# Optimization experiments

Measured on AMD Instinct MI355X. Metric: run time of the kernel, lower is better.

Reference implementation:

```python
import jax, jax.numpy as jnp
import numpy as np

T, B, DIM, N, K = 512, 32, 1024, 256, 32  # K = checkpoint interval, divides T


def setup_inputs() -> dict:
    key = jax.random.key(0)
    k1, k2, k3, k4 = jax.random.split(key, 4)
    scale = 1.0 / np.sqrt(DIM)  # keep projections O(1) like trained weights
    return {
        "x": jax.random.normal(k1, (T, B, DIM), dtype=jnp.float32),
        "S0": jnp.zeros((B, N, N), dtype=jnp.float32),
        "W_k": jax.random.normal(k2, (N, DIM), dtype=jnp.float32) * scale,
        "W_v": jax.random.normal(k3, (N, DIM), dtype=jnp.float32) * scale,
        "W_q": jax.random.normal(k4, (N, DIM), dtype=jnp.float32) * scale,
    }


def reference(x, S0, W_k, W_v, W_q):
    # Projections (batched GEMMs), done once up-front as in the torch code.
    k_all = jnp.einsum("tbd,nd->tbn", x, W_k)
    v_all = jnp.einsum("tbd,nd->tbn", x, W_v)
    q_all = jnp.einsum("tbd,nd->tbn", x, W_q)
    k_norm = k_all / (jnp.linalg.norm(k_all, axis=-1, keepdims=True) + 1e-6)

    def step(S, kvq):
        kn, v, q = kvq  # each [B, N]
        retrieved = jnp.einsum("bij,bj->bi", S, kn)          # S @ k_norm
        S = S + (v - retrieved)[:, :, None] * kn[:, None, :]  # rank-1 delta write
        Sq = jnp.einsum("bij,bj->bi", S, q)                   # readout with updated S
        out = Sq * jax.nn.silu(Sq)
        return S, out

    def segment(S, kvq_seg):
        return jax.lax.scan(step, S, kvq_seg)

    nseg = T // K
    seg_kvq = (
        k_norm.reshape(nseg, K, B, N),
        v_all.reshape(nseg, K, B, N),
        q_all.reshape(nseg, K, B, N),
    )
    _, outs = jax.lax.scan(segment, S0, seg_kvq)  # [nseg, K, B, N]
    return outs.reshape(T, B, N)
```

## Files before the change

kernel.cpp:

```cpp
#include <hip/hip_runtime.h>
#include <hip/hip_bf16.h>
#include <math.h>

#define T_DIM 512
#define B_DIM 32
#define D_DIM 1024
#define N_DIM 256
#define M_DIM (T_DIM * B_DIM)
#define CHUNK 32
#define NCHUNK (T_DIM / CHUNK)
#define IBLK 32
#define ST (B_DIM * N_DIM)
#define BK 32

typedef _Float16 f16;
typedef _Float16 f16x8 __attribute__((ext_vector_type(8)));
typedef _Float16 f16x4 __attribute__((ext_vector_type(4)));
typedef __fp16   h16x2 __attribute__((ext_vector_type(2)));
typedef float    f32x4 __attribute__((ext_vector_type(4)));

#define LDK 264
#define LDT 40
#define LDV 36

#define GLOAD_LDS16(g, l)                                         \
  __builtin_amdgcn_global_load_lds(                               \
      (const __attribute__((address_space(1))) void*)(g),         \
      (__attribute__((address_space(3))) void*)(l), 16, 0, 0)

__device__ __forceinline__ f16x8 cvt8(const float4& a, const float4& b) {
  f16x8 h;
  h[0] = (f16)a.x; h[1] = (f16)a.y; h[2] = (f16)a.z; h[3] = (f16)a.w;
  h[4] = (f16)b.x; h[5] = (f16)b.y; h[6] = (f16)b.z; h[7] = (f16)b.w;
  return h;
}

__device__ __forceinline__ f16x8 pk8(const f32x4 a, const f32x4 b) {
  union { f16x8 v; h16x2 p[4]; } u;
  u.p[0] = __builtin_amdgcn_cvt_pkrtz(a[0], a[1]);
  u.p[1] = __builtin_amdgcn_cvt_pkrtz(a[2], a[3]);
  u.p[2] = __builtin_amdgcn_cvt_pkrtz(b[0], b[1]);
  u.p[3] = __builtin_amdgcn_cvt_pkrtz(b[2], b[3]);
  return u.v;
}

__global__ __launch_bounds__(256) void cvt_w_kernel(
    const float* __restrict__ wk, const float* __restrict__ wv,
    const float* __restrict__ wq, f16* __restrict__ out) {
  const int i = (blockIdx.x * 256 + threadIdx.x) * 8;
  const int m = blockIdx.y;
  const float* src = (m == 0) ? wk : (m == 1) ? wv : wq;
  const float4 f0 = *(const float4*)(src + i);
  const float4 f1 = *(const float4*)(src + i + 4);
  *(f16x8*)(out + (size_t)m * (N_DIM * D_DIM) + i) = cvt8(f0, f1);
}

__global__ __launch_bounds__(256, 4) void proj_gemm_mfma(
    const float* __restrict__ x, const f16* __restrict__ Wh,
    f16* __restrict__ ok, f16* __restrict__ ov, f16* __restrict__ oq) {
  __shared__ __align__(16) float Af[128 * BK];
  __shared__ __align__(16) f16   Bh[128 * BK];

  const int tid  = threadIdx.x;
  const int lane = tid & 63;
  const int w    = tid >> 6;
  const int wm   = w >> 1, wn = w & 1;
  const int lr   = lane & 15;
  const int lq   = lane >> 4;

  const int mb  = blockIdx.x * 128;
  const int mat = blockIdx.y >> 1;
  const int nb  = (blockIdx.y & 1) * 128;

  const f16* Wmat = Wh + (size_t)mat * (N_DIM * D_DIM) + (size_t)nb * D_DIM;
  f16*       C    = (mat == 0) ? ok : (mat == 1) ? ov : oq;

  const int arow = 8 * w + (lane >> 3);
  const int acq  = (lane & 7) ^ (lane >> 3);
  const int brow = 16 * w + (lane >> 2);
  const int bco  = (lane & 3) ^ ((lane >> 3) & 3);

  const float* a_base = x + (size_t)mb * D_DIM;

  f32x4 acc[4][4];
  #pragma unroll
  for (int i = 0; i < 4; ++i)
    #pragma unroll
    for (int j = 0; j < 4; ++j) acc[i][j] = (f32x4){0.f, 0.f, 0.f, 0.f};

  for (int kt = 0; kt < D_DIM; kt += BK) {
    #pragma unroll
    for (int j = 0; j < 4; ++j) {
      const int r = 32 * j + arow;
      GLOAD_LDS16(a_base + (size_t)r * D_DIM + kt + acq * 4,
                  &Af[(32 * j + 8 * w) * BK]);
    }
    #pragma unroll
    for (int j = 0; j < 2; ++j) {
      const int r = 64 * j + brow;
      GLOAD_LDS16(Wmat + (size_t)r * D_DIM + kt + bco * 8,
                  &Bh[(64 * j + 16 * w) * BK]);
    }
    __syncthreads();

    f16x8 af[4], bf[4];
    #pragma unroll
    for (int mi = 0; mi < 4; ++mi) {
      const int row = 64 * wm + 16 * mi + lr;
      const int q0  = (2 * lq)     ^ (row & 7);
      const int q1  = (2 * lq + 1) ^ (row & 7);
      const f32x4 a0 = *(const f32x4*)&Af[row * BK + q0 * 4];
      const f32x4 a1 = *(const f32x4*)&Af[row * BK + q1 * 4];
      af[mi] = pk8(a0, a1);
    }
    #pragma unroll
    for (int nj = 0; nj < 4; ++nj) {
      const int row = 64 * wn + 16 * nj + lr;
      const int sp  = lq ^ ((lr >> 1) & 3);
      bf[nj] = *(const f16x8*)&Bh[row * BK + sp * 8];
    }
    #pragma unroll
    for (int mi = 0; mi < 4; ++mi)
      #pragma unroll
      for (int nj = 0; nj < 4; ++nj)
        acc[mi][nj] = __builtin_amdgcn_mfma_f32_16x16x32_f16(af[mi], bf[nj], acc[mi][nj], 0, 0, 0);
    __syncthreads();
  }

  #pragma unroll
  for (int mi = 0; mi < 4; ++mi)
    #pragma unroll
    for (int nj = 0; nj < 4; ++nj)
      #pragma unroll
      for (int r = 0; r < 4; ++r) {
        const int rg = mb + 64 * wm + 16 * mi + 4 * lq + r;
        const int cg = nb + 64 * wn + 16 * nj + lr;
        C[(size_t)rg * N_DIM + cg] = (f16)acc[mi][nj][r];
      }
}

__global__ __launch_bounds__(256) void knorm_kernel(f16* __restrict__ k) {
  const int w    = threadIdx.x >> 6;
  const int lane = threadIdx.x & 63;
  const int row  = blockIdx.x * 4 + w;
  f16* p = k + (size_t)row * N_DIM + lane * 4;
  f16x4 h = *reinterpret_cast<const f16x4*>(p);
  const float x0 = (float)h[0], x1 = (float)h[1], x2 = (float)h[2], x3 = (float)h[3];
  float ss = x0 * x0 + x1 * x1 + x2 * x2 + x3 * x3;
  #pragma unroll
  for (int m = 1; m < 64; m <<= 1) ss += __shfl_xor(ss, m, 64);
  const float inv = 1.0f / (sqrtf(ss) + 1e-6f);
  h[0] = (f16)(x0 * inv); h[1] = (f16)(x1 * inv);
  h[2] = (f16)(x2 * inv); h[3] = (f16)(x3 * inv);
  *reinterpret_cast<f16x4*>(p) = h;
}

__global__ __launch_bounds__(256, 2) void precompute_wg(
    const f16* __restrict__ kn, const f16* __restrict__ q,
    f16* __restrict__ Wg, f16* __restrict__ Gg, f16* __restrict__ KTg) {
  __shared__ __align__(16) f16 Kh[32 * LDK];
  __shared__ __align__(16) f16 Qh[32 * LDK];
  __shared__ float Al[32 * 33];

  const int tid  = threadIdx.x;
  const int lane = tid & 63;
  const int w    = tid >> 6;
  const int lr   = lane & 15;
  const int lq   = lane >> 4;
  const int tm   = w >> 1, tn = w & 1;
  const int b    = blockIdx.x >> 4;
  const int c    = blockIdx.x & 15;
  const int t0g  = c * CHUNK;

  {
    const int t = tid >> 3, cg = tid & 7;
    const f16* ks = kn + (size_t)(t0g + t) * ST + b * N_DIM + cg * 32;
    const f16* qs = q  + (size_t)(t0g + t) * ST + b * N_DIM + cg * 32;
    #pragma unroll
    for (int m = 0; m < 4; ++m) {
      *(f16x8*)&Kh[t * LDK + cg * 32 + 8 * m] = ((const f16x8*)ks)[m];
      *(f16x8*)&Qh[t * LDK + cg * 32 + 8 * m] = ((const f16x8*)qs)[m];
    }
  }
  __syncthreads();

  {
    f16* kt_dst = KTg + ((size_t)blockIdx.x * N_DIM + tid) * CHUNK;
    #pragma unroll
    for (int t8 = 0; t8 < 4; ++t8) {
      f16x8 h;
      #pragma unroll
      for (int e = 0; e < 8; ++e) h[e] = Kh[(8 * t8 + e) * LDK + tid];
      *(f16x8*)(kt_dst + 8 * t8) = h;
    }
  }

  f32x4 Aa = {0.f, 0.f, 0.f, 0.f}, Ga = {0.f, 0.f, 0.f, 0.f};
  #pragma unroll
  for (int kk = 0; kk < 8; ++kk) {
    f16x8 ka = *(const f16x8*)&Kh[(16 * tm + lr) * LDK + 32 * kk + 8 * lq];
    f16x8 qa = *(const f16x8*)&Qh[(16 * tm + lr) * LDK + 32 * kk + 8 * lq];
    f16x8 kb = *(const f16x8*)&Kh[(16 * tn + lr) * LDK + 32 * kk + 8 * lq];
    Aa = __builtin_amdgcn_mfma_f32_16x16x32_f16(ka, kb, Aa, 0, 0, 0);
    Ga = __builtin_amdgcn_mfma_f32_16x16x32_f16(qa, kb, Ga, 0, 0, 0);
  }
  {
    const int s = 16 * tn + lr;
    f16* gdst = Gg + (size_t)blockIdx.x * 1280;
    #pragma unroll
    for (int r = 0; r < 4; ++r) {
      const int t = 16 * tm + 4 * lq + r;
      Al[t * 33 + s] = (s < t) ? Aa[r] : 0.f;
      gdst[t * LDT + s] = (f16)((s <= t) ? Ga[r] : 0.f);
    }
  }
  __syncthreads();

  if (tid < 32) {
    float wv[32];
    f16* wdst = Wg + (size_t)blockIdx.x * 1280;
    #pragma unroll
    for (int t = 0; t < 32; ++t) {
      float s0 = 0.f, s1 = 0.f, s2 = 0.f, s3 = 0.f;
      #pragma unroll
      for (int s = 0; s < 32; ++s) {
        if (s >= t) break;
        const float a = Al[t * 33 + s];
        if ((s & 3) == 0) s0 = fmaf(a, wv[s], s0);
        else if ((s & 3) == 1) s1 = fmaf(a, wv[s], s1);
        else if ((s & 3) == 2) s2 = fmaf(a, wv[s], s2);
        else s3 = fmaf(a, wv[s], s3);
      }
      wv[t] = ((t == tid) ? 1.f : 0.f) - ((s0 + s1) + (s2 + s3));
    }
    #pragma unroll
    for (int t = 0; t < 32; ++t) wdst[t * LDT + tid] = (f16)wv[t];
  }
}

__global__ __launch_bounds__(256, 1) void scan_chunked(
    const f16* __restrict__ kn, const f16* __restrict__ v,
    const f16* __restrict__ q, const float* __restrict__ S0,
    const f16* __restrict__ Wg, const f16* __restrict__ Gg,
    const f16* __restrict__ KTg, float* __restrict__ out) {
  __shared__ __align__(16) f16 Kh[32 * LDK];
  __shared__ __align__(16) f16 Qh[32 * LDK];
  __shared__ __align__(16) f16 Sh[32 * LDK];
  __shared__ __align__(16) f16 KhT[256 * LDT];
  __shared__ __align__(16) f16 Wl[32 * LDT];
  __shared__ __align__(16) f16 Gl[32 * LDT];
  __shared__ __align__(16) f16 U0T[32 * LDT];
  __shared__ __align__(16) f16 UT[32 * LDT];
  __shared__ __align__(16) float Vl[32 * LDV];

  const int tid  = threadIdx.x;
  const int lane = tid & 63;
  const int w    = tid >> 6;
  const int lr   = lane & 15;
  const int lq   = lane >> 4;
  const int tm   = w >> 1, tn = w & 1;
  const int b    = blockIdx.x & 31;
  const int i0   = (blockIdx.x >> 5) * IBLK;

  f32x4 acc[2][4];
  const float* S0b = S0 + (size_t)b * N_DIM * N_DIM + (size_t)i0 * N_DIM;
  #pragma unroll
  for (int ti = 0; ti < 2; ++ti)
    #pragma unroll
    for (int jt = 0; jt < 4; ++jt)
      #pragma unroll
      for (int r = 0; r < 4; ++r) {
        const int i = 16 * ti + 4 * lq + r;
        const int j = 64 * w + 16 * jt + lr;
        acc[ti][jt][r] = S0b[(size_t)i * N_DIM + j];
      }
  {
    const int i = tid >> 3, cg = tid & 7;
    const float* ss = S0b + (size_t)i * N_DIM + cg * 32;
    #pragma unroll
    for (int m = 0; m < 4; ++m) {
      float4 f0 = *(const float4*)(ss + 8 * m);
      float4 f1 = *(const float4*)(ss + 8 * m + 4);
      *(f16x8*)&Sh[i * LDK + cg * 32 + 8 * m] = cvt8(f0, f1);
    }
  }
  __syncthreads();

  for (int c = 0; c < NCHUNK; ++c) {
    const int t0g = c * CHUNK;
    {
      const int t = tid >> 3, cg = tid & 7;
      const f16* ks = kn + (size_t)(t0g + t) * ST + b * N_DIM + cg * 32;
      const f16* qs = q  + (size_t)(t0g + t) * ST + b * N_DIM + cg * 32;
      #pragma unroll
      for (int m = 0; m < 4; ++m) {
        *(f16x8*)&Kh[t * LDK + cg * 32 + 8 * m] = ((const f16x8*)ks)[m];
        *(f16x8*)&Qh[t * LDK + cg * 32 + 8 * m] = ((const f16x8*)qs)[m];
      }
      const f16x4 vf = *(const f16x4*)(v + (size_t)(t0g + t) * ST + b * N_DIM + i0 + cg * 4);
      *(float4*)&Vl[t * LDV + cg * 4] =
          make_float4((float)vf[0], (float)vf[1], (float)vf[2], (float)vf[3]);
    }
    {
      const f16* src = KTg + ((size_t)(b * NCHUNK + c) * N_DIM + tid) * CHUNK;
      #pragma unroll
      for (int m = 0; m < 4; ++m)
        *(f16x8*)&KhT[tid * LDT + 8 * m] = ((const f16x8*)src)[m];
    }
    if (tid < 160) {
      const f16x8* wsrc = (const f16x8*)(Wg + (size_t)(b * NCHUNK + c) * 1280);
      const f16x8* gsrc = (const f16x8*)(Gg + (size_t)(b * NCHUNK + c) * 1280);
      ((f16x8*)Wl)[tid] = wsrc[tid];
      ((f16x8*)Gl)[tid] = gsrc[tid];
    }
    __syncthreads();

    f32x4 Pacc = {0.f, 0.f, 0.f, 0.f};
    f32x4 Oq   = {0.f, 0.f, 0.f, 0.f};
    #pragma unroll
    for (int kk = 0; kk < 8; ++kk) {
      f16x8 ka = *(const f16x8*)&Kh[(16 * tm + lr) * LDK + 32 * kk + 8 * lq];
      f16x8 qa = *(const f16x8*)&Qh[(16 * tm + lr) * LDK + 32 * kk + 8 * lq];
      f16x8 sb = *(const f16x8*)&Sh[(16 * tn + lr) * LDK + 32 * kk + 8 * lq];
      Pacc = __builtin_amdgcn_mfma_f32_16x16x32_f16(ka, sb, Pacc, 0, 0, 0);
      Oq   = __builtin_amdgcn_mfma_f32_16x16x32_f16(qa, sb, Oq,   0, 0, 0);
    }
    {
      const int i = 16 * tn + lr;
      const int t0 = 16 * tm + 4 * lq;
      f16x4 u0;
      #pragma unroll
      for (int r = 0; r < 4; ++r) u0[r] = (f16)(Vl[(t0 + r) * LDV + i] - Pacc[r]);
      *(f16x4*)&U0T[i * LDT + t0] = u0;
    }
    __syncthreads();

    {
      f16x8 wa = *(const f16x8*)&Wl[(16 * tm + lr) * LDT + 8 * lq];
      f16x8 ub = *(const f16x8*)&U0T[(16 * tn + lr) * LDT + 8 * lq];
      f32x4 z = {0.f, 0.f, 0.f, 0.f};
      f32x4 Ud = __builtin_amdgcn_mfma_f32_16x16x32_f16(wa, ub, z, 0, 0, 0);
      const int i = 16 * tn + lr;
      const int t0 = 16 * tm + 4 * lq;
      f16x4 uh;
      #pragma unroll
      for (int r = 0; r < 4; ++r) uh[r] = (f16)Ud[r];
      *(f16x4*)&UT[i * LDT + t0] = uh;
    }
    __syncthreads();

    {
      f16x8 ga = *(const f16x8*)&Gl[(16 * tm + lr) * LDT + 8 * lq];
      f16x8 ub = *(const f16x8*)&UT[(16 * tn + lr) * LDT + 8 * lq];
      f32x4 O = __builtin_amdgcn_mfma_f32_16x16x32_f16(ga, ub, Oq, 0, 0, 0);
      const int i = 16 * tn + lr;
      const int tt0 = 16 * tm + 4 * lq;
      #pragma unroll
      for (int r = 0; r < 4; ++r) {
        const float sq = O[r];
        const float sig = 1.0f / (1.0f + __expf(-sq));
        out[(size_t)(t0g + tt0 + r) * ST + b * N_DIM + i0 + i] = sq * sq * sig;
      }
    }
    #pragma unroll
    for (int ti = 0; ti < 2; ++ti) {
      f16x8 ua = *(const f16x8*)&UT[(16 * ti + lr) * LDT + 8 * lq];
      #pragma unroll
      for (int jt = 0; jt < 4; ++jt) {
        f16x8 kb = *(const f16x8*)&KhT[(64 * w + 16 * jt + lr) * LDT + 8 * lq];
        acc[ti][jt] = __builtin_amdgcn_mfma_f32_16x16x32_f16(ua, kb, acc[ti][jt], 0, 0, 0);
      }
    }
    #pragma unroll
    for (int ti = 0; ti < 2; ++ti)
      #pragma unroll
      for (int jt = 0; jt < 4; ++jt)
        #pragma unroll
        for (int r = 0; r < 4; ++r)
          Sh[(16 * ti + 4 * lq + r) * LDK + 64 * w + 16 * jt + lr] = (f16)acc[ti][jt][r];
    __syncthreads();
  }
}

extern "C" void kernel_launch(void* const* d_in, const int* in_sizes, int n_in,
                              void* d_out, int out_size, void* d_ws, size_t ws_size,
                              hipStream_t stream) {
  (void)in_sizes; (void)n_in; (void)out_size; (void)ws_size;
  const float* x  = (const float*)d_in[0];
  const float* S0 = (const float*)d_in[1];
  const float* Wk = (const float*)d_in[2];
  const float* Wv = (const float*)d_in[3];
  const float* Wq = (const float*)d_in[4];
  float* outp = (float*)d_out;

  f16* kn  = (f16*)d_ws;
  f16* vv  = kn + (size_t)M_DIM * N_DIM;
  f16* qq  = vv + (size_t)M_DIM * N_DIM;
  f16* Wg  = qq + (size_t)M_DIM * N_DIM;
  f16* Gg  = Wg + (size_t)B_DIM * NCHUNK * 1280;
  f16* KTg = Gg + (size_t)B_DIM * NCHUNK * 1280;
  f16* Wh  = KTg + (size_t)B_DIM * NCHUNK * N_DIM * CHUNK;

  dim3 gw(N_DIM * D_DIM / 8 / 256, 3);
  cvt_w_kernel<<<gw, 256, 0, stream>>>(Wk, Wv, Wq, Wh);
  dim3 gg(M_DIM / 128, 6);
  proj_gemm_mfma<<<gg, 256, 0, stream>>>(x, Wh, kn, vv, qq);
  knorm_kernel<<<M_DIM / 4, 256, 0, stream>>>(kn);
  precompute_wg<<<B_DIM * NCHUNK, 256, 0, stream>>>(kn, qq, Wg, Gg, KTg);
  scan_chunked<<<B_DIM * (N_DIM / IBLK), 256, 0, stream>>>(kn, vv, qq, S0, Wg, Gg, KTg, outp);
}
```

Measured before the change: 108.4 us.

## Convert A tile to fp16 in registers and double K-tile depth in projection GEMM

The projection GEMM now loads x through registers, converts it to fp16 before writing to LDS, and stores an fp16 A tile instead of an fp32 one. BK doubles to 64, so each barrier pair covers two MFMA k-substeps, and a new XOR swizzle is applied to both tiles. The aim is to cut LDS footprint and read traffic for A and halve the number of sync iterations. The cost is that A loads no longer go directly global-to-LDS, more registers are used, and the occupancy hint drops to 3.

```diff
diff --git a/kernel.cpp b/kernel.cpp
--- a/kernel.cpp
+++ b/kernel.cpp
@@ -11,7 +11,7 @@
 #define NCHUNK (T_DIM / CHUNK)
 #define IBLK 32
 #define ST (B_DIM * N_DIM)
-#define BK 32
+#define BK 64
 
 typedef _Float16 f16;
 typedef _Float16 f16x8 __attribute__((ext_vector_type(8)));
@@ -35,12 +35,10 @@
   return h;
 }
 
-__device__ __forceinline__ f16x8 pk8(const f32x4 a, const f32x4 b) {
-  union { f16x8 v; h16x2 p[4]; } u;
-  u.p[0] = __builtin_amdgcn_cvt_pkrtz(a[0], a[1]);
-  u.p[1] = __builtin_amdgcn_cvt_pkrtz(a[2], a[3]);
-  u.p[2] = __builtin_amdgcn_cvt_pkrtz(b[0], b[1]);
-  u.p[3] = __builtin_amdgcn_cvt_pkrtz(b[2], b[3]);
+__device__ __forceinline__ f16x4 pk4(const float4 a) {
+  union { f16x4 v; h16x2 p[2]; } u;
+  u.p[0] = __builtin_amdgcn_cvt_pkrtz(a.x, a.y);
+  u.p[1] = __builtin_amdgcn_cvt_pkrtz(a.z, a.w);
   return u.v;
 }
 
@@ -55,11 +53,11 @@
   *(f16x8*)(out + (size_t)m * (N_DIM * D_DIM) + i) = cvt8(f0, f1);
 }
 
-__global__ __launch_bounds__(256, 4) void proj_gemm_mfma(
+__global__ __launch_bounds__(256, 3) void proj_gemm_mfma(
     const float* __restrict__ x, const f16* __restrict__ Wh,
     f16* __restrict__ ok, f16* __restrict__ ov, f16* __restrict__ oq) {
-  __shared__ __align__(16) float Af[128 * BK];
-  __shared__ __align__(16) f16   Bh[128 * BK];
+  __shared__ __align__(16) f16 Ah[128 * BK];
+  __shared__ __align__(16) f16 Bh[128 * BK];
 
   const int tid  = threadIdx.x;
   const int lane = tid & 63;
@@ -75,12 +73,10 @@
   const f16* Wmat = Wh + (size_t)mat * (N_DIM * D_DIM) + (size_t)nb * D_DIM;
   f16*       C    = (mat == 0) ? ok : (mat == 1) ? ov : oq;
 
-  const int arow = 8 * w + (lane >> 3);
-  const int acq  = (lane & 7) ^ (lane >> 3);
-  const int brow = 16 * w + (lane >> 2);
-  const int bco  = (lane & 3) ^ ((lane >> 3) & 3);
-
-  const float* a_base = x + (size_t)mb * D_DIM;
+  const int arb = 32 * w + (lane >> 4);
+  const int aq  = lane & 15;
+  const int br0 = 8 * w + (lane >> 3);
+  const int bsl = lane & 7;
 
   f32x4 acc[4][4];
   #pragma unroll
@@ -89,41 +85,45 @@
     for (int j = 0; j < 4; ++j) acc[i][j] = (f32x4){0.f, 0.f, 0.f, 0.f};
 
   for (int kt = 0; kt < D_DIM; kt += BK) {
+    float4 areg[8];
+    #pragma unroll
+    for (int m = 0; m < 8; ++m)
+      areg[m] = *(const float4*)(x + (size_t)(mb + arb + 4 * m) * D_DIM + kt + aq * 4);
     #pragma unroll
     for (int j = 0; j < 4; ++j) {
-      const int r = 32 * j + arow;
-      GLOAD_LDS16(a_base + (size_t)r * D_DIM + kt + acq * 4,
-                  &Af[(32 * j + 8 * w) * BK]);
-    }
-    #pragma unroll
-    for (int j = 0; j < 2; ++j) {
-      const int r = 64 * j + brow;
-      GLOAD_LDS16(Wmat + (size_t)r * D_DIM + kt + bco * 8,
-                  &Bh[(64 * j + 16 * w) * BK]);
-    }
-    __syncthreads();
-
-    f16x8 af[4], bf[4];
-    #pragma unroll
-    for (int mi = 0; mi < 4; ++mi) {
-      const int row = 64 * wm + 16 * mi + lr;
-      const int q0  = (2 * lq)     ^ (row & 7);
-      const int q1  = (2 * lq + 1) ^ (row & 7);
-      const f32x4 a0 = *(const f32x4*)&Af[row * BK + q0 * 4];
-      const f32x4 a1 = *(const f32x4*)&Af[row * BK + q1 * 4];
-      af[mi] = pk8(a0, a1);
-    }
-    #pragma unroll
-    for (int nj = 0; nj < 4; ++nj) {
-      const int row = 64 * wn + 16 * nj + lr;
-      const int sp  = lq ^ ((lr >> 1) & 3);
-      bf[nj] = *(const f16x8*)&Bh[row * BK + sp * 8];
-    }
-    #pragma unroll
-    for (int mi = 0; mi < 4; ++mi)
-      #pragma unroll
-      for (int nj = 0; nj < 4; ++nj)
-        acc[mi][nj] = __builtin_amdgcn_mfma_f32_16x16x32_f16(af[mi], bf[nj], acc[mi][nj], 0, 0, 0);
+      const int r = 32 * j + br0;
+      GLOAD_LDS16(Wmat + (size_t)r * D_DIM + kt + (bsl ^ (r & 7)) * 8,
+                  &Bh[(32 * j + 8 * w) * BK]);
+    }
+    #pragma unroll
+    for (int m = 0; m < 8; ++m) {
+      const int row = arb + 4 * m;
+      const int s   = (aq >> 1) ^ (row & 7);
+      *(f16x4*)&Ah[row * BK + s * 8 + (aq & 1) * 4] = pk4(areg[m]);
+    }
+    __syncthreads();
+
+    #pragma unroll
+    for (int kk = 0; kk < 2; ++kk) {
+      f16x8 af[4], bf[4];
+      #pragma unroll
+      for (int mi = 0; mi < 4; ++mi) {
+        const int row = 64 * wm + 16 * mi + lr;
+        const int sp  = (4 * kk + lq) ^ (row & 7);
+        af[mi] = *(const f16x8*)&Ah[row * BK + sp * 8];
+      }
+      #pragma unroll
+      for (int nj = 0; nj < 4; ++nj) {
+        const int row = 64 * wn + 16 * nj + lr;
+        const int sp  = (4 * kk + lq) ^ (row & 7);
+        bf[nj] = *(const f16x8*)&Bh[row * BK + sp * 8];
+      }
+      #pragma unroll
+      for (int mi = 0; mi < 4; ++mi)
+        #pragma unroll
+        for (int nj = 0; nj < 4; ++nj)
+          acc[mi][nj] = __builtin_amdgcn_mfma_f32_16x16x32_f16(af[mi], bf[nj], acc[mi][nj], 0, 0, 0);
+    }
     __syncthreads();
   }
 
```

After: 123.2 us. 1.14x slower.

## Double-buffer LDS tiles in projection GEMM to overlap loads with MFMA

Applied to the files above, without the earlier changes.

Projection GEMM tiles for x and W now live in two LDS buffers. The next K-slice is prefetched into the spare buffer while the current one is read and fed to MFMA, which removes one barrier per iteration. The hope is to hide global-to-LDS latency behind compute. In exchange, LDS use doubles and the occupancy hint drops from 4 to 3 blocks per CU. The XOR swizzle on the B tile is also dropped, which may bring back LDS bank conflicts on B fragment reads.

```diff
diff --git a/kernel.cpp b/kernel.cpp
--- a/kernel.cpp
+++ b/kernel.cpp
@@ -55,11 +55,11 @@
   *(f16x8*)(out + (size_t)m * (N_DIM * D_DIM) + i) = cvt8(f0, f1);
 }
 
-__global__ __launch_bounds__(256, 4) void proj_gemm_mfma(
+__global__ __launch_bounds__(256, 3) void proj_gemm_mfma(
     const float* __restrict__ x, const f16* __restrict__ Wh,
     f16* __restrict__ ok, f16* __restrict__ ov, f16* __restrict__ oq) {
-  __shared__ __align__(16) float Af[128 * BK];
-  __shared__ __align__(16) f16   Bh[128 * BK];
+  __shared__ __align__(16) float Af[2][128 * BK];
+  __shared__ __align__(16) f16   Bh[2][128 * BK];
 
   const int tid  = threadIdx.x;
   const int lane = tid & 63;
@@ -75,12 +75,10 @@
   const f16* Wmat = Wh + (size_t)mat * (N_DIM * D_DIM) + (size_t)nb * D_DIM;
   f16*       C    = (mat == 0) ? ok : (mat == 1) ? ov : oq;
 
-  const int arow = 8 * w + (lane >> 3);
-  const int acq  = (lane & 7) ^ (lane >> 3);
-  const int brow = 16 * w + (lane >> 2);
-  const int bco  = (lane & 3) ^ ((lane >> 3) & 3);
-
-  const float* a_base = x + (size_t)mb * D_DIM;
+  const int ar  = lane >> 3;
+  const int acq = (lane & 7) ^ ar;
+  const int brr = lane >> 2;
+  const int bco = lane & 3;
 
   f32x4 acc[4][4];
   #pragma unroll
@@ -88,43 +86,58 @@
     #pragma unroll
     for (int j = 0; j < 4; ++j) acc[i][j] = (f32x4){0.f, 0.f, 0.f, 0.f};
 
+  #pragma unroll
+  for (int j = 0; j < 4; ++j) {
+    const int r = 32 * j + 8 * w + ar;
+    GLOAD_LDS16(x + (size_t)(mb + r) * D_DIM + acq * 4, &Af[0][(32 * j + 8 * w) * BK]);
+  }
+  #pragma unroll
+  for (int j = 0; j < 2; ++j) {
+    const int r = 64 * j + 16 * w + brr;
+    GLOAD_LDS16(Wmat + (size_t)r * D_DIM + bco * 8, &Bh[0][(64 * j + 16 * w) * BK]);
+  }
+  __syncthreads();
+
+  int cur = 0;
   for (int kt = 0; kt < D_DIM; kt += BK) {
-    #pragma unroll
-    for (int j = 0; j < 4; ++j) {
-      const int r = 32 * j + arow;
-      GLOAD_LDS16(a_base + (size_t)r * D_DIM + kt + acq * 4,
-                  &Af[(32 * j + 8 * w) * BK]);
-    }
-    #pragma unroll
-    for (int j = 0; j < 2; ++j) {
-      const int r = 64 * j + brow;
-      GLOAD_LDS16(Wmat + (size_t)r * D_DIM + kt + bco * 8,
-                  &Bh[(64 * j + 16 * w) * BK]);
+    if (kt + BK < D_DIM) {
+      #pragma unroll
+      for (int j = 0; j < 4; ++j) {
+        const int r = 32 * j + 8 * w + ar;
+        GLOAD_LDS16(x + (size_t)(mb + r) * D_DIM + kt + BK + acq * 4,
+                    &Af[cur ^ 1][(32 * j + 8 * w) * BK]);
+      }
+      #pragma unroll
+      for (int j = 0; j < 2; ++j) {
+        const int r = 64 * j + 16 * w + brr;
+        GLOAD_LDS16(Wmat + (size_t)r * D_DIM + kt + BK + bco * 8,
+                    &Bh[cur ^ 1][(64 * j + 16 * w) * BK]);
+      }
+    }
+    {
+      f16x8 af[4], bf[4];
+      #pragma unroll
+      for (int mi = 0; mi < 4; ++mi) {
+        const int row = 64 * wm + 16 * mi + lr;
+        const int q0  = (2 * lq)     ^ (row & 7);
+        const int q1  = (2 * lq + 1) ^ (row & 7);
+        const f32x4 a0 = *(const f32x4*)&Af[cur][row * BK + q0 * 4];
+        const f32x4 a1 = *(const f32x4*)&Af[cur][row * BK + q1 * 4];
+        af[mi] = pk8(a0, a1);
+      }
+      #pragma unroll
+      for (int nj = 0; nj < 4; ++nj) {
+        const int row = 64 * wn + 16 * nj + lr;
+        bf[nj] = *(const f16x8*)&Bh[cur][row * BK + lq * 8];
+      }
+      #pragma unroll
+      for (int mi = 0; mi < 4; ++mi)
+        #pragma unroll
+        for (int nj = 0; nj < 4; ++nj)
+          acc[mi][nj] = __builtin_amdgcn_mfma_f32_16x16x32_f16(af[mi], bf[nj], acc[mi][nj], 0, 0, 0);
     }
     __syncthreads();
-
-    f16x8 af[4], bf[4];
-    #pragma unroll
-    for (int mi = 0; mi < 4; ++mi) {
-      const int row = 64 * wm + 16 * mi + lr;
-      const int q0  = (2 * lq)     ^ (row & 7);
-      const int q1  = (2 * lq + 1) ^ (row & 7);
-      const f32x4 a0 = *(const f32x4*)&Af[row * BK + q0 * 4];
-      const f32x4 a1 = *(const f32x4*)&Af[row * BK + q1 * 4];
-      af[mi] = pk8(a0, a1);
-    }
-    #pragma unroll
-    for (int nj = 0; nj < 4; ++nj) {
-      const int row = 64 * wn + 16 * nj + lr;
-      const int sp  = lq ^ ((lr >> 1) & 3);
-      bf[nj] = *(const f16x8*)&Bh[row * BK + sp * 8];
-    }
-    #pragma unroll
-    for (int mi = 0; mi < 4; ++mi)
-      #pragma unroll
-      for (int nj = 0; nj < 4; ++nj)
-        acc[mi][nj] = __builtin_amdgcn_mfma_f32_16x16x32_f16(af[mi], bf[nj], acc[mi][nj], 0, 0, 0);
-    __syncthreads();
+    cur ^= 1;
   }
 
   #pragma unroll
```

Measured after the change: 108.6 us. About the same (+0.2%).
